# Kernel tuning notes

Measured on AMD Instinct MI355X. Metric: run time of the kernel, lower is better.

Reference implementation:

```python
import jax, jax.numpy as jnp
import numpy as np

# --- config (Qwen3-Next linear attention defaults) ---
B, S, H = 1, 256, 2048
NK, NV, DK, DV, K = 4, 32, 128, 128, 4
KEY_DIM = NK * DK          # 512
VAL_DIM = NV * DV          # 4096
CONV_DIM = 2 * KEY_DIM + VAL_DIM  # 5120
EPS = 1e-6


def setup_inputs() -> dict:
    key = jax.random.key(0)
    ks = jax.random.split(key, 8)
    rn = lambda k, shape, sc: jax.random.normal(k, shape, jnp.float32) * sc
    return {
        "hidden_states": jax.random.normal(ks[0], (B, S, H), jnp.float32),
        "w_qkvz": rn(ks[1], (2 * KEY_DIM + 2 * VAL_DIM, H), 0.02),  # in_proj_qkvz weight
        "w_ba": rn(ks[2], (2 * NV, H), 0.02),                        # in_proj_ba weight
        "w_out": rn(ks[3], (H, VAL_DIM), 0.02),                      # out_proj weight
        "conv_w": rn(ks[4], (CONV_DIM, 1, K), 0.1),                  # depthwise conv weight [C,1,K]
        "dt_bias": jnp.ones((NV,), jnp.float32),
        "A_log": jnp.zeros((NV,), jnp.float32),
        "norm_w": jnp.ones((DV,), jnp.float32),
    }


def reference(hidden_states, w_qkvz, w_ba, w_out, conv_w, dt_bias, A_log, norm_w):
    b, s, _ = hidden_states.shape
    # input projections (Linear without bias: x @ W.T)
    qkvz = hidden_states @ w_qkvz.T                      # [B,S,9216]
    ba = hidden_states @ w_ba.T                          # [B,S,64]
    q, k, v, z = jnp.split(qkvz, [KEY_DIM, 2 * KEY_DIM, 2 * KEY_DIM + VAL_DIM], axis=-1)
    beta, alpha = jnp.split(ba, 2, axis=-1)              # each [B,S,NV]

    # causal depthwise conv over concat(q,k,v), then silu
    qkv = jnp.concatenate([q, k, v], axis=-1).transpose(0, 2, 1)   # [B,C,S]
    qkv = jax.lax.conv_general_dilated(
        qkv, conv_w, window_strides=(1,), padding=[(K - 1, 0)],
        dimension_numbers=("NCH", "OIH", "NCH"), feature_group_count=CONV_DIM)
    qkv = jax.nn.silu(qkv).transpose(0, 2, 1)            # [B,S,C]
    q, k, v = jnp.split(qkv, [KEY_DIM, 2 * KEY_DIM], axis=-1)

    q = q.reshape(b, s, NK, DK)
    k = k.reshape(b, s, NK, DK)
    v = v.reshape(b, s, NV, DV)
    z = z.reshape(b, s, NV, DV)

    # GQA-style head expansion (repeat_interleave)
    ratio = NV // NK
    q = jnp.repeat(q, ratio, axis=2)                     # [B,S,NV,DK]
    k = jnp.repeat(k, ratio, axis=2)

    # NOTE: original computes g = -softplus(-A_log - alpha) but never uses it (dead code).
    beta_g = jax.nn.sigmoid(beta + dt_bias)[..., None]   # [B,S,NV,1]
    q = q * (DK ** -0.5)

    # naive delta-rule: full outer-product tensor + cumsum (memory-bound)
    kv = jnp.einsum("bsnk,bsnv->bsnkv", k, v * beta_g)   # [B,S,NV,DK,DV]
    out = jnp.einsum("bsnk,bsnkv->bsnv", q, jnp.cumsum(kv, axis=1))  # [B,S,NV,DV]

    # gated RMSNorm over head_v_dim in fp32
    of = out.astype(jnp.float32)
    var = jnp.mean(of * of, axis=-1, keepdims=True)
    of = of * jax.lax.rsqrt(var + EPS) * norm_w
    of = of * jax.nn.silu(z.astype(jnp.float32))

    return of.reshape(b, s, VAL_DIM) @ w_out.T           # [B,S,H]
```

## Files before the change

kernel.cpp:

```cpp
#include <hip/hip_runtime.h>
#include <hip/hip_bf16.h>

#define S_LEN   256
#define HID     2048
#define NVH     32
#define DKD     128
#define DVD     128
#define KEYDIM  512
#define VALDIM  4096
#define CONVDIM 5120
#define QKVZ_N  9216
#define EPS_F   1e-6f

typedef __attribute__((ext_vector_type(8))) short bf16x8;
typedef __attribute__((ext_vector_type(4))) float f32x4;

__device__ __forceinline__ unsigned short f2bf(float f) {
    union { float f; unsigned int i; } v; v.f = f;
    unsigned int x = v.i;
    return (unsigned short)((x + 0x7FFFu + ((x >> 16) & 1u)) >> 16);
}
__device__ __forceinline__ unsigned int pk2(float x, float y) {
    union { __hip_bfloat162 h; unsigned int u; } c;
    c.h = __float22bfloat162_rn(float2{x, y});
    return c.u;
}
__device__ __forceinline__ float4 asf4(uint4 u) {
    union { uint4 u; float4 f; } c; c.u = u; return c.f;
}
__device__ __forceinline__ uint4 cvt8_pack(float4 a, float4 b) {
    uint4 r;
    r.x = pk2(a.x, a.y); r.y = pk2(a.z, a.w);
    r.z = pk2(b.x, b.y); r.w = pk2(b.z, b.w);
    return r;
}

template<bool A_F32>
__global__ __launch_bounds__(256, 2)
void gemm_tile(const void* __restrict__ Ap, const float* __restrict__ B,
               float* __restrict__ Cpart, int N, int K, int kc) {
    __shared__ __align__(16) unsigned short As[128][72];
    __shared__ __align__(16) unsigned short Bs[128][72];

    const int tid  = threadIdx.x;
    const int lane = tid & 63, wave = tid >> 6;
    const int wm = wave >> 1, wn = wave & 1;
    const int quad = lane >> 4, l16 = lane & 15;
    const int m0 = blockIdx.y * 128, n0 = blockIdx.x * 128;
    const int kbeg = blockIdx.z * kc;
    const int niter = kc >> 6;

    const int lc = (tid & 7) << 3;
    const int lr = tid >> 3;

    f32x4 acc[4][4];
#pragma unroll
    for (int i = 0; i < 4; i++)
#pragma unroll
        for (int j = 0; j < 4; j++) acc[i][j] = (f32x4){0.f, 0.f, 0.f, 0.f};

    uint4 qa[8], qb[8];

    auto ld_tiles = [&](int kk) {
        if constexpr (A_F32) {
            const float* a = (const float*)Ap + (size_t)(m0 + lr) * K + kk + lc;
#pragma unroll
            for (int i = 0; i < 4; i++) {
                qa[2 * i]     = *(const uint4*)(a + (size_t)(32 * i) * K);
                qa[2 * i + 1] = *(const uint4*)(a + (size_t)(32 * i) * K + 4);
            }
        } else {
            const unsigned short* a = (const unsigned short*)Ap + (size_t)(m0 + lr) * K + kk + lc;
#pragma unroll
            for (int i = 0; i < 4; i++)
                qa[i] = *(const uint4*)(a + (size_t)(32 * i) * K);
        }
        const float* b = B + (size_t)(n0 + lr) * K + kk + lc;
#pragma unroll
        for (int i = 0; i < 4; i++) {
            qb[2 * i]     = *(const uint4*)(b + (size_t)(32 * i) * K);
            qb[2 * i + 1] = *(const uint4*)(b + (size_t)(32 * i) * K + 4);
        }
    };
    auto st_tiles = [&]() {
#pragma unroll
        for (int i = 0; i < 4; i++) {
            if constexpr (A_F32)
                *(uint4*)(&As[lr + 32 * i][lc]) = cvt8_pack(asf4(qa[2 * i]), asf4(qa[2 * i + 1]));
            else
                *(uint4*)(&As[lr + 32 * i][lc]) = qa[i];
            *(uint4*)(&Bs[lr + 32 * i][lc]) = cvt8_pack(asf4(qb[2 * i]), asf4(qb[2 * i + 1]));
        }
    };

    ld_tiles(kbeg);
    st_tiles();
    __syncthreads();

    for (int it = 0; it < niter; ++it) {
        if (it + 1 < niter) ld_tiles(kbeg + (it + 1) * 64);

        bf16x8 af[2][4], bfr[2][4];
#pragma unroll
        for (int t = 0; t < 4; t++) {
#pragma unroll
            for (int ks = 0; ks < 2; ks++) {
                af[ks][t]  = *(const bf16x8*)(&As[wm * 64 + t * 16 + l16][ks * 32 + quad * 8]);
                bfr[ks][t] = *(const bf16x8*)(&Bs[wn * 64 + t * 16 + l16][ks * 32 + quad * 8]);
            }
        }
#pragma unroll
        for (int ks = 0; ks < 2; ks++)
#pragma unroll
            for (int i = 0; i < 4; i++)
#pragma unroll
                for (int j = 0; j < 4; j++)
                    acc[i][j] = __builtin_amdgcn_mfma_f32_16x16x32_bf16(af[ks][i], bfr[ks][j], acc[i][j], 0, 0, 0);

        if (it + 1 < niter) {
            __syncthreads();
            st_tiles();
            __syncthreads();
        }
    }

    float* C = Cpart + (size_t)blockIdx.z * 256 * N;
#pragma unroll
    for (int i = 0; i < 4; i++)
#pragma unroll
        for (int j = 0; j < 4; j++)
#pragma unroll
            for (int r = 0; r < 4; r++) {
                int row = m0 + wm * 64 + i * 16 + quad * 4 + r;
                int col = n0 + wn * 64 + j * 16 + l16;
                C[(size_t)row * N + col] = acc[i][j][r];
            }
}

template<int P>
__global__ void reduce_sum(const float* __restrict__ part, float* __restrict__ out, int n) {
    int i = (blockIdx.x * 256 + threadIdx.x) * 4;
    if (i >= n) return;
    float4 s = *(const float4*)(part + i);
#pragma unroll
    for (int p = 1; p < P; p++) {
        float4 v = *(const float4*)(part + (size_t)p * n + i);
        s.x += v.x; s.y += v.y; s.z += v.z; s.w += v.w;
    }
    *(float4*)(out + i) = s;
}

__global__ void ba_proj(const float* __restrict__ hs,
                        const float* __restrict__ w_ba,
                        float* __restrict__ ba) {
    int s = blockIdx.x, n = threadIdx.x;
    const float* x = hs + (size_t)s * HID;
    const float* w = w_ba + (size_t)n * HID;
    float acc = 0.f;
    for (int k = 0; k < HID; k += 4) {
        float4 xv = *(const float4*)(x + k);
        float4 wv = *(const float4*)(w + k);
        acc += xv.x * wv.x + xv.y * wv.y + xv.z * wv.z + xv.w * wv.w;
    }
    ba[s * 64 + n] = acc;
}

__global__ void conv_silu(const float* __restrict__ qkvz,
                          const float* __restrict__ conv_w,
                          float* __restrict__ out) {
    int idx = blockIdx.x * blockDim.x + threadIdx.x;
    if (idx >= S_LEN * CONVDIM) return;
    int s = idx / CONVDIM, c = idx % CONVDIM;
    float acc = 0.f;
#pragma unroll
    for (int j = 0; j < 4; j++) {
        int t = s - 3 + j;
        if (t >= 0) acc += qkvz[(size_t)t * QKVZ_N + c] * conv_w[c * 4 + j];
    }
    out[idx] = acc / (1.f + __expf(-acc));
}

__global__ __launch_bounds__(256)
void scores_k(const float* __restrict__ conv, const float* __restrict__ ba,
              const float* __restrict__ dt_bias, float* __restrict__ scores) {
    if (blockIdx.x > blockIdx.y) return;
    int hk = blockIdx.z;
    int s0 = blockIdx.y * 16, t0 = blockIdx.x * 16;
    __shared__ float Qs[16][132], Ks[16][132];
    int tid = threadIdx.x;
    int qoff = hk * DKD;
    int koff = KEYDIM + hk * DKD;
    for (int idx = tid; idx < 16 * 128; idx += 256) {
        int i = idx >> 7, d = idx & 127;
        Qs[i][d] = conv[(size_t)(s0 + i) * CONVDIM + qoff + d];
        Ks[i][d] = conv[(size_t)(t0 + i) * CONVDIM + koff + d];
    }
    __syncthreads();
    int tx = tid & 15, ty = tid >> 4;
    int s = s0 + ty, t = t0 + tx;
    float dot = 0.f;
    for (int d = 0; d < 128; d++) dot += Qs[ty][d] * Ks[tx][d];
    float base = (t <= s) ? dot * 0.08838834764831845f : 0.f;
#pragma unroll
    for (int v = 0; v < 8; v++) {
        int n = hk * 8 + v;
        float b = ba[t * 64 + n] + dt_bias[n];
        float bg = 1.f / (1.f + __expf(-b));
        scores[((size_t)n * 256 + s) * 256 + t] = base * bg;
    }
}

__global__ __launch_bounds__(256)
void attn_v(const float* __restrict__ scores, const float* __restrict__ conv,
            float* __restrict__ attn) {
    int n = blockIdx.z, s0 = blockIdx.y * 16, d0 = blockIdx.x * 16;
    int voff = 2 * KEYDIM + n * DVD;
    __shared__ float Ss[16][16], Vs[16][17];
    int tid = threadIdx.x, dx = tid & 15, sy = tid >> 4;
    float acc = 0.f;
    for (int t0 = 0; t0 <= s0; t0 += 16) {
        Ss[sy][dx] = scores[((size_t)n * 256 + s0 + sy) * 256 + t0 + dx];
        Vs[sy][dx] = conv[(size_t)(t0 + sy) * CONVDIM + voff + d0 + dx];
        __syncthreads();
#pragma unroll
        for (int j = 0; j < 16; j++) acc += Ss[sy][j] * Vs[j][dx];
        __syncthreads();
    }
    attn[((size_t)(s0 + sy) * NVH + n) * DVD + d0 + dx] = acc;
}

__global__ __launch_bounds__(128)
void rmsnorm_gate(const float* __restrict__ attn, const float* __restrict__ qkvz,
                  const float* __restrict__ norm_w,
                  unsigned short* __restrict__ normed) {
    int s = blockIdx.x >> 5, n = blockIdx.x & 31;
    int d = threadIdx.x;
    float x = attn[((size_t)s * NVH + n) * DVD + d];
    float sq = x * x;
#pragma unroll
    for (int off = 32; off > 0; off >>= 1) sq += __shfl_down(sq, off, 64);
    __shared__ float parts[2];
    if ((d & 63) == 0) parts[d >> 6] = sq;
    __syncthreads();
    float ms = (parts[0] + parts[1]) * (1.f / 128.f);
    float inv = rsqrtf(ms + EPS_F);
    float z = qkvz[(size_t)s * QKVZ_N + CONVDIM + n * DVD + d];
    float sz = z / (1.f + __expf(-z));
    float v = x * inv * norm_w[d] * sz;
    normed[((size_t)s * NVH + n) * DVD + d] = f2bf(v);
}

extern "C" void kernel_launch(void* const* d_in, const int* in_sizes, int n_in,
                              void* d_out, int out_size, void* d_ws, size_t ws_size,
                              hipStream_t stream) {
    const float* hs      = (const float*)d_in[0];
    const float* w_qkvz  = (const float*)d_in[1];
    const float* w_ba    = (const float*)d_in[2];
    const float* w_out   = (const float*)d_in[3];
    const float* conv_w  = (const float*)d_in[4];
    const float* dt_bias = (const float*)d_in[5];
    const float* norm_w  = (const float*)d_in[7];

    char* ws = (char*)d_ws;
    float* qkvz   = (float*)ws;          ws += (size_t)S_LEN * QKVZ_N * 4;
    float* ba     = (float*)ws;          ws += (size_t)S_LEN * 64 * 4;
    float* conv   = (float*)ws;          ws += (size_t)S_LEN * CONVDIM * 4;
    float* scores = (float*)ws;          ws += (size_t)NVH * S_LEN * S_LEN * 4;
    float* attn   = (float*)ws;          ws += (size_t)S_LEN * VALDIM * 4;
    unsigned short* normed = (unsigned short*)ws; ws += (size_t)S_LEN * VALDIM * 2;
    float* scratch = (float*)ws;

    gemm_tile<true><<<dim3(QKVZ_N / 128, 2, 2), 256, 0, stream>>>(hs, w_qkvz, scratch, QKVZ_N, HID, HID / 2);
    ba_proj<<<S_LEN, 64, 0, stream>>>(hs, w_ba, ba);
    reduce_sum<2><<<(S_LEN * QKVZ_N) / 1024, 256, 0, stream>>>(scratch, qkvz, S_LEN * QKVZ_N);
    conv_silu<<<(S_LEN * CONVDIM) / 256, 256, 0, stream>>>(qkvz, conv_w, conv);
    scores_k<<<dim3(16, 16, 4), 256, 0, stream>>>(conv, ba, dt_bias, scores);
    attn_v<<<dim3(8, 16, NVH), 256, 0, stream>>>(scores, conv, attn);
    rmsnorm_gate<<<S_LEN * NVH, 128, 0, stream>>>(attn, qkvz, norm_w, normed);
    gemm_tile<false><<<dim3(HID / 128, 2, 8), 256, 0, stream>>>(normed, w_out, scratch, HID, VALDIM, VALDIM / 8);
    reduce_sum<8><<<(S_LEN * HID) / 1024, 256, 0, stream>>>(scratch, (float*)d_out, S_LEN * HID);
}
```

Measured before the change: 296.2 us.

## Raise split-K via aliased workspace, widen attn_v tiles, split ba_proj reduction

The workspace is re-laid out so the two GEMM split-K scratch buffers alias buffers that are not live at the same time. When the workspace is large enough, this doubles the split-K factor of both projection GEMMs, giving more blocks and better CU fill at the cost of more partial-sum traffic in reduce_sum. attn_v now has each block cover the full 128-wide value head, using float4 loads and 8 accumulators per thread, which cuts the grid from 4096 to 512 blocks. ba_proj splits its K loop across four wavefronts and combines the partial sums through shared memory.

```diff
diff --git a/kernel.cpp b/kernel.cpp
--- a/kernel.cpp
+++ b/kernel.cpp
@@ -150,19 +150,27 @@
     *(float4*)(out + i) = s;
 }
 
-__global__ void ba_proj(const float* __restrict__ hs,
-                        const float* __restrict__ w_ba,
-                        float* __restrict__ ba) {
-    int s = blockIdx.x, n = threadIdx.x;
-    const float* x = hs + (size_t)s * HID;
-    const float* w = w_ba + (size_t)n * HID;
+__global__ __launch_bounds__(256)
+void ba_proj(const float* __restrict__ hs,
+             const float* __restrict__ w_ba,
+             float* __restrict__ ba) {
+    int s = blockIdx.x;
+    int n = threadIdx.x & 63, seg = threadIdx.x >> 6;
+    const float* x = hs + (size_t)s * HID + seg * 512;
+    const float* w = w_ba + (size_t)n * HID + seg * 512;
     float acc = 0.f;
-    for (int k = 0; k < HID; k += 4) {
+#pragma unroll 4
+    for (int k = 0; k < 512; k += 4) {
         float4 xv = *(const float4*)(x + k);
         float4 wv = *(const float4*)(w + k);
         acc += xv.x * wv.x + xv.y * wv.y + xv.z * wv.z + xv.w * wv.w;
     }
-    ba[s * 64 + n] = acc;
+    __shared__ float parts[4][64];
+    parts[seg][n] = acc;
+    __syncthreads();
+    if (threadIdx.x < 64)
+        ba[s * 64 + threadIdx.x] = parts[0][threadIdx.x] + parts[1][threadIdx.x]
+                                 + parts[2][threadIdx.x] + parts[3][threadIdx.x];
 }
 
 __global__ void conv_silu(const float* __restrict__ qkvz,
@@ -213,20 +221,29 @@
 __global__ __launch_bounds__(256)
 void attn_v(const float* __restrict__ scores, const float* __restrict__ conv,
             float* __restrict__ attn) {
-    int n = blockIdx.z, s0 = blockIdx.y * 16, d0 = blockIdx.x * 16;
+    int n = blockIdx.y, s0 = blockIdx.x * 16;
     int voff = 2 * KEYDIM + n * DVD;
-    __shared__ float Ss[16][16], Vs[16][17];
-    int tid = threadIdx.x, dx = tid & 15, sy = tid >> 4;
-    float acc = 0.f;
+    __shared__ float Ss[16][17];
+    __shared__ float Vs[16][132];
+    int tid = threadIdx.x, sy = tid >> 4, dx = tid & 15;
+    float acc[8] = {0.f, 0.f, 0.f, 0.f, 0.f, 0.f, 0.f, 0.f};
     for (int t0 = 0; t0 <= s0; t0 += 16) {
         Ss[sy][dx] = scores[((size_t)n * 256 + s0 + sy) * 256 + t0 + dx];
-        Vs[sy][dx] = conv[(size_t)(t0 + sy) * CONVDIM + voff + d0 + dx];
+        const float* vp = conv + (size_t)(t0 + sy) * CONVDIM + voff + dx * 8;
+        *(float4*)&Vs[sy][dx * 8]     = *(const float4*)vp;
+        *(float4*)&Vs[sy][dx * 8 + 4] = *(const float4*)(vp + 4);
         __syncthreads();
 #pragma unroll
-        for (int j = 0; j < 16; j++) acc += Ss[sy][j] * Vs[j][dx];
+        for (int j = 0; j < 16; j++) {
+            float sv = Ss[sy][j];
+#pragma unroll
+            for (int r = 0; r < 8; r++) acc[r] += sv * Vs[j][dx + 16 * r];
+        }
         __syncthreads();
     }
-    attn[((size_t)(s0 + sy) * NVH + n) * DVD + d0 + dx] = acc;
+    float* op = attn + ((size_t)(s0 + sy) * NVH + n) * DVD;
+#pragma unroll
+    for (int r = 0; r < 8; r++) op[dx + 16 * r] = acc[r];
 }
 
 __global__ __launch_bounds__(128)
@@ -262,21 +279,29 @@
     const float* norm_w  = (const float*)d_in[7];
 
     char* ws = (char*)d_ws;
-    float* qkvz   = (float*)ws;          ws += (size_t)S_LEN * QKVZ_N * 4;
-    float* ba     = (float*)ws;          ws += (size_t)S_LEN * 64 * 4;
-    float* conv   = (float*)ws;          ws += (size_t)S_LEN * CONVDIM * 4;
-    float* scores = (float*)ws;          ws += (size_t)NVH * S_LEN * S_LEN * 4;
-    float* attn   = (float*)ws;          ws += (size_t)S_LEN * VALDIM * 4;
-    unsigned short* normed = (unsigned short*)ws; ws += (size_t)S_LEN * VALDIM * 2;
-    float* scratch = (float*)ws;
-
-    gemm_tile<true><<<dim3(QKVZ_N / 128, 2, 2), 256, 0, stream>>>(hs, w_qkvz, scratch, QKVZ_N, HID, HID / 2);
-    ba_proj<<<S_LEN, 64, 0, stream>>>(hs, w_ba, ba);
-    reduce_sum<2><<<(S_LEN * QKVZ_N) / 1024, 256, 0, stream>>>(scratch, qkvz, S_LEN * QKVZ_N);
+    float* qkvz = (float*)ws;  ws += (size_t)S_LEN * QKVZ_N * 4;
+    float* ba   = (float*)ws;  ws += (size_t)S_LEN * 64 * 4;
+    float* conv = (float*)ws;  ws += (size_t)S_LEN * CONVDIM * 4;
+    char* regB = ws;
+    float* scratch1 = (float*)regB;
+    unsigned short* normed = (unsigned short*)regB;
+    float* scratch2 = (float*)(regB + 2097152);
+    float* attn   = (float*)(regB + 2097152);
+    float* scores = (float*)(regB + 2097152 + 4194304);
+
+    const bool big = ws_size >= (size_t)54 * 1024 * 1024;
+    const int sk1 = big ? 4 : 2;
+    const int sk2 = big ? 16 : 8;
+
+    gemm_tile<true><<<dim3(QKVZ_N / 128, 2, sk1), 256, 0, stream>>>(hs, w_qkvz, scratch1, QKVZ_N, HID, HID / sk1);
+    ba_proj<<<S_LEN, 256, 0, stream>>>(hs, w_ba, ba);
+    if (big) reduce_sum<4><<<(S_LEN * QKVZ_N) / 1024, 256, 0, stream>>>(scratch1, qkvz, S_LEN * QKVZ_N);
+    else     reduce_sum<2><<<(S_LEN * QKVZ_N) / 1024, 256, 0, stream>>>(scratch1, qkvz, S_LEN * QKVZ_N);
     conv_silu<<<(S_LEN * CONVDIM) / 256, 256, 0, stream>>>(qkvz, conv_w, conv);
     scores_k<<<dim3(16, 16, 4), 256, 0, stream>>>(conv, ba, dt_bias, scores);
-    attn_v<<<dim3(8, 16, NVH), 256, 0, stream>>>(scores, conv, attn);
+    attn_v<<<dim3(16, NVH), 256, 0, stream>>>(scores, conv, attn);
     rmsnorm_gate<<<S_LEN * NVH, 128, 0, stream>>>(attn, qkvz, norm_w, normed);
-    gemm_tile<false><<<dim3(HID / 128, 2, 8), 256, 0, stream>>>(normed, w_out, scratch, HID, VALDIM, VALDIM / 8);
-    reduce_sum<8><<<(S_LEN * HID) / 1024, 256, 0, stream>>>(scratch, (float*)d_out, S_LEN * HID);
-}
+    gemm_tile<false><<<dim3(HID / 128, 2, sk2), 256, 0, stream>>>(normed, w_out, scratch2, HID, VALDIM, VALDIM / sk2);
+    if (big) reduce_sum<16><<<(S_LEN * HID) / 1024, 256, 0, stream>>>(scratch2, (float*)d_out, S_LEN * HID);
+    else     reduce_sum<8><<<(S_LEN * HID) / 1024, 256, 0, stream>>>(scratch2, (float*)d_out, S_LEN * HID);
+}
```

Result: faster. 274.5 us (-7.3%).
